# Kernel tuning notes

Measured on AMD Instinct MI355X. Metric: run time of the kernel, lower is better.

Reference implementation:

```python
import jax, jax.numpy as jnp
import numpy as np


def _dense_image_warp(img, flow):
    """Faithful port of tfa.image.dense_image_warp (bilinear interpolate_bilinear).
    img:  [B,H,W,C] float
    flow: [B,H,W,2] float, output[b,h,w] = img sampled at (h - flow[...,0], w - flow[...,1])
    """
    B, H, W, C = img.shape
    grid_y = jnp.arange(H, dtype=img.dtype)[None, :, None]   # [1,H,1]
    grid_x = jnp.arange(W, dtype=img.dtype)[None, None, :]   # [1,1,W]
    qy = grid_y - flow[..., 0]  # [B,H,W] query rows
    qx = grid_x - flow[..., 1]  # [B,H,W] query cols

    # tfa interpolate_bilinear: floor clipped to [0, size-2], alpha clipped to [0,1]
    fy = jnp.clip(jnp.floor(qy), 0.0, H - 2)
    fx = jnp.clip(jnp.floor(qx), 0.0, W - 2)
    ay = jnp.clip(qy - fy, 0.0, 1.0)[..., None]  # [B,H,W,1]
    ax = jnp.clip(qx - fx, 0.0, 1.0)[..., None]
    iy = fy.astype(jnp.int32)
    ix = fx.astype(jnp.int32)

    b = jnp.arange(B, dtype=jnp.int32)[:, None, None]  # [B,1,1] broadcast over H,W
    top_left     = img[b, iy,     ix]      # [B,H,W,C]
    top_right    = img[b, iy,     ix + 1]
    bottom_left  = img[b, iy + 1, ix]
    bottom_right = img[b, iy + 1, ix + 1]

    interp_top    = top_left + ax * (top_right - top_left)
    interp_bottom = bottom_left + ax * (bottom_right - bottom_left)
    return interp_top + ay * (interp_bottom - interp_top)


def setup_inputs() -> dict:
    key = jax.random.key(0)
    k1, k2 = jax.random.split(key)
    B, H, W, C = 8, 512, 512, 16
    x = jax.random.normal(k1, (B, H, W, C), dtype=jnp.float32)
    # scale flow so displacements span a realistic few-pixel range
    flow = jax.random.normal(k2, (B, H, W, 2), dtype=jnp.float32) * 5.0
    return {"x": x, "flow": flow}


def reference(x, flow):
    return _dense_image_warp(x, flow)
```

## Files before the change

### kernel.cpp

```cpp
#include <hip/hip_runtime.h>


constexpr int B = 8;
constexpr int H = 512;
constexpr int W = 512;
constexpr int C = 16;

__global__ __launch_bounds__(256) void warp_kernel(
    const float* __restrict__ img,
    const float* __restrict__ flow,
    float* __restrict__ out)
{
    const int tid = blockIdx.x * blockDim.x + threadIdx.x;
    const int p  = tid >> 2;
    const int c0 = (tid & 3) << 2;

    const int w = p & (W - 1);
    const int h = (p >> 9) & (H - 1);
    const int b = p >> 18;

    const float2 f = *reinterpret_cast<const float2*>(flow + 2 * (size_t)p);

    const float qy = (float)h - f.x;
    const float qx = (float)w - f.y;

    float fy = fminf(fmaxf(floorf(qy), 0.0f), (float)(H - 2));
    float fx = fminf(fmaxf(floorf(qx), 0.0f), (float)(W - 2));
    const float ay = fminf(fmaxf(qy - fy, 0.0f), 1.0f);
    const float ax = fminf(fmaxf(qx - fx, 0.0f), 1.0f);
    const int iy = (int)fy;
    const int ix = (int)fx;

    const size_t rowStride = (size_t)W * C;
    const float* base = img + ((size_t)((b * H + iy) * W + ix) * C + c0);

    const float4 tl = *reinterpret_cast<const float4*>(base);
    const float4 tr = *reinterpret_cast<const float4*>(base + C);
    const float4 bl = *reinterpret_cast<const float4*>(base + rowStride);
    const float4 br = *reinterpret_cast<const float4*>(base + rowStride + C);

    float4 o;
    {
        const float t0 = tl.x + ax * (tr.x - tl.x);
        const float b0 = bl.x + ax * (br.x - bl.x);
        o.x = t0 + ay * (b0 - t0);
    }
    {
        const float t1 = tl.y + ax * (tr.y - tl.y);
        const float b1 = bl.y + ax * (br.y - bl.y);
        o.y = t1 + ay * (b1 - t1);
    }
    {
        const float t2 = tl.z + ax * (tr.z - tl.z);
        const float b2 = bl.z + ax * (br.z - bl.z);
        o.z = t2 + ay * (b2 - t2);
    }
    {
        const float t3 = tl.w + ax * (tr.w - tl.w);
        const float b3 = bl.w + ax * (br.w - bl.w);
        o.w = t3 + ay * (b3 - t3);
    }

    *reinterpret_cast<float4*>(out + (size_t)p * C + c0) = o;
}

extern "C" void kernel_launch(void* const* d_in, const int* in_sizes, int n_in,
                              void* d_out, int out_size, void* d_ws, size_t ws_size,
                              hipStream_t stream) {
    const float* img  = (const float*)d_in[0];
    const float* flow = (const float*)d_in[1];
    float* out = (float*)d_out;

    const int total = B * H * W * 4;
    const int block = 256;
    const int grid = total / block;
    warp_kernel<<<grid, block, 0, stream>>>(img, flow, out);
}
```

Before: 253.2 us.

## Use eight lanes per pixel with shuffles to share neighbor texels and flow

```diff
diff --git a/kernel.cpp b/kernel.cpp
--- a/kernel.cpp
+++ b/kernel.cpp
@@ -12,17 +12,22 @@
     float* __restrict__ out)
 {
     const int tid = blockIdx.x * blockDim.x + threadIdx.x;
-    const int p  = tid >> 2;
-    const int c0 = (tid & 3) << 2;
+    const int p = tid >> 3;
+    const int j = tid & 7;
 
     const int w = p & (W - 1);
     const int h = (p >> 9) & (H - 1);
     const int b = p >> 18;
 
-    const float2 f = *reinterpret_cast<const float2*>(flow + 2 * (size_t)p);
+    float2 f = make_float2(0.0f, 0.0f);
+    if (j == 0) {
+        f = *reinterpret_cast<const float2*>(flow + 2 * (size_t)p);
+    }
+    const float fy_flow = __shfl(f.x, 0, 8);
+    const float fx_flow = __shfl(f.y, 0, 8);
 
-    const float qy = (float)h - f.x;
-    const float qx = (float)w - f.y;
+    const float qy = (float)h - fy_flow;
+    const float qx = (float)w - fx_flow;
 
     float fy = fminf(fmaxf(floorf(qy), 0.0f), (float)(H - 2));
     float fx = fminf(fmaxf(floorf(qx), 0.0f), (float)(W - 2));
@@ -31,37 +36,46 @@
     const int iy = (int)fy;
     const int ix = (int)fx;
 
-    const size_t rowStride = (size_t)W * C;
-    const float* base = img + ((size_t)((b * H + iy) * W + ix) * C + c0);
+    const int rowStride = W * C;
+    const float* rowT = img + ((b * H + iy) * W + ix) * C + j * 4;
 
-    const float4 tl = *reinterpret_cast<const float4*>(base);
-    const float4 tr = *reinterpret_cast<const float4*>(base + C);
-    const float4 bl = *reinterpret_cast<const float4*>(base + rowStride);
-    const float4 br = *reinterpret_cast<const float4*>(base + rowStride + C);
+    const float4 top = *reinterpret_cast<const float4*>(rowT);
+    const float4 bot = *reinterpret_cast<const float4*>(rowT + rowStride);
 
-    float4 o;
-    {
-        const float t0 = tl.x + ax * (tr.x - tl.x);
-        const float b0 = bl.x + ax * (br.x - bl.x);
-        o.x = t0 + ay * (b0 - t0);
+    float4 topo, boto;
+    topo.x = __shfl_xor(top.x, 4);
+    topo.y = __shfl_xor(top.y, 4);
+    topo.z = __shfl_xor(top.z, 4);
+    topo.w = __shfl_xor(top.w, 4);
+    boto.x = __shfl_xor(bot.x, 4);
+    boto.y = __shfl_xor(bot.y, 4);
+    boto.z = __shfl_xor(bot.z, 4);
+    boto.w = __shfl_xor(bot.w, 4);
+
+    if (j < 4) {
+        float4 o;
+        {
+            const float t0 = top.x + ax * (topo.x - top.x);
+            const float b0 = bot.x + ax * (boto.x - bot.x);
+            o.x = t0 + ay * (b0 - t0);
+        }
+        {
+            const float t1 = top.y + ax * (topo.y - top.y);
+            const float b1 = bot.y + ax * (boto.y - bot.y);
+            o.y = t1 + ay * (b1 - t1);
+        }
+        {
+            const float t2 = top.z + ax * (topo.z - top.z);
+            const float b2 = bot.z + ax * (boto.z - bot.z);
+            o.z = t2 + ay * (b2 - t2);
+        }
+        {
+            const float t3 = top.w + ax * (topo.w - top.w);
+            const float b3 = bot.w + ax * (boto.w - bot.w);
+            o.w = t3 + ay * (b3 - t3);
+        }
+        *reinterpret_cast<float4*>(out + (size_t)p * C + j * 4) = o;
     }
-    {
-        const float t1 = tl.y + ax * (tr.y - tl.y);
-        const float b1 = bl.y + ax * (br.y - bl.y);
-        o.y = t1 + ay * (b1 - t1);
-    }
-    {
-        const float t2 = tl.z + ax * (tr.z - tl.z);
-        const float b2 = bl.z + ax * (br.z - bl.z);
-        o.z = t2 + ay * (b2 - t2);
-    }
-    {
-        const float t3 = tl.w + ax * (tr.w - tl.w);
-        const float b3 = bl.w + ax * (br.w - bl.w);
-        o.w = t3 + ay * (b3 - t3);
-    }
-
-    *reinterpret_cast<float4*>(out + (size_t)p * C + c0) = o;
 }
 
 extern "C" void kernel_launch(void* const* d_in, const int* in_sizes, int n_in,
@@ -71,7 +85,7 @@
     const float* flow = (const float*)d_in[1];
     float* out = (float*)d_out;
 
-    const int total = B * H * W * 4;
+    const int total = B * H * W * 8;
     const int block = 256;
     const int grid = total / block;
     warp_kernel<<<grid, block, 0, stream>>>(img, flow, out);
```

New measurement: 262.3 us. +3.6%, slower.
